# Kernel tuning notes

Hardware: AMD Instinct MI355X
Metric: run time of the kernel (lower is better)

The kernel has to match this reference:

```python
import jax, jax.numpy as jnp
import numpy as np

EPS = 1e-07      # epsilon from init kwargs
LRELU = 0.1      # LeakyReLU negative slope
LEVEL = 0        # level 0 -> _cond_inter: i%2!=0 and j%2!=0


def _conv_circ(x, w, b):
    # circular-padded 2D conv, NCHW / OIHW
    p = w.shape[-1] // 2
    x = jnp.pad(x, ((0, 0), (0, 0), (p, p), (p, p)), mode='wrap')
    y = jax.lax.conv_general_dilated(x, w, (1, 1), 'VALID',
                                     dimension_numbers=('NCHW', 'OIHW', 'NCHW'))
    return y + b[None, :, None, None]


def _net(x, w1, b1, w2, b2, w3, b3):
    h = jax.nn.leaky_relu(_conv_circ(x, w1, b1), LRELU)
    h = jax.nn.leaky_relu(_conv_circ(h, w2, b2), LRELU)
    return jax.nn.sigmoid(_conv_circ(h, w3, b3))


def _positions(L):
    ii, jj = np.meshgrid(np.arange(L), np.arange(L), indexing='ij')
    if LEVEL == 0:
        mask = (ii % 2 != 0) & (jj % 2 != 0)
    else:
        mask = ((ii % 2 == 0) & (jj % 2 != 0)) | ((ii % 2 != 0) & (jj % 2 == 0))
    # row-major order matches the nested python loop
    return jnp.asarray(np.stack([ii[mask], jj[mask]], axis=1), dtype=jnp.int32)  # [S,2]


def setup_inputs() -> dict:
    key = jax.random.key(0)
    ks = jax.random.split(key, 7)
    B, L, H, K = 4096, 16, 32, 5
    x = jnp.where(jax.random.normal(ks[0], (B, 1, L, L)) > 0, 1.0, -1.0).astype(jnp.float32)
    w1 = (jax.random.normal(ks[1], (H, 1, K, K)) * 0.1).astype(jnp.float32)
    b1 = jnp.zeros((H,), jnp.float32)
    w2 = (jax.random.normal(ks[2], (H, H, K, K)) * 0.05).astype(jnp.float32)
    b2 = jnp.zeros((H,), jnp.float32)
    w3 = (jax.random.normal(ks[3], (1, H, K, K)) * 0.05).astype(jnp.float32)
    b3 = jnp.zeros((1,), jnp.float32)
    return {'x': x, 'w1': w1, 'b1': b1, 'w2': w2, 'b2': b2, 'w3': w3, 'b3': b3}


def reference(x, w1, b1, w2, b2, w3, b3):
    B, L = x.shape[0], x.shape[-1]
    pos = _positions(L)                                   # [S,2] static positions
    keys = jax.random.split(jax.random.key(42), pos.shape[0])

    def step(carry, inp):
        x, logq = carry
        ij, k = inp
        i, j = ij[0], ij[1]
        x_hat = _net(x, w1, b1, w2, b2, w3, b3)           # full CNN pass per pixel
        p = x_hat[:, 0, i, j]                             # [B]
        samp = jax.lax.stop_gradient(
            jnp.where(jax.random.uniform(k, (B,)) < p, 1.0, -1.0))  # bernoulli*2-1
        x = x.at[:, 0, i, j].set(samp)
        xb = (samp + 1.0) * 0.5
        logq = logq + jnp.log(p + EPS) * xb + jnp.log(1.0 - p + EPS) * (1.0 - xb)
        return (x, logq), None

    (x, logq), _ = jax.lax.scan(step, (x, jnp.zeros((B,), x.dtype)), (pos, keys))
    return x, logq
```

## Files before the change

### kernel.cpp

```cpp
#include <hip/hip_runtime.h>
#include <cstdint>


struct U2 { uint32_t x, y; };

__device__ __forceinline__ U2 tf2x32(uint32_t k0, uint32_t k1, uint32_t x0, uint32_t x1) {
  uint32_t k2 = k0 ^ k1 ^ 0x1BD11BDAu;
#define TFROT(r) { x0 += x1; x1 = (x1 << (r)) | (x1 >> (32 - (r))); x1 ^= x0; }
  x0 += k0; x1 += k1;
  TFROT(13) TFROT(15) TFROT(26) TFROT(6)
  x0 += k1; x1 += k2 + 1u;
  TFROT(17) TFROT(29) TFROT(16) TFROT(24)
  x0 += k2; x1 += k0 + 2u;
  TFROT(13) TFROT(15) TFROT(26) TFROT(6)
  x0 += k0; x1 += k1 + 3u;
  TFROT(17) TFROT(29) TFROT(16) TFROT(24)
  x0 += k1; x1 += k2 + 4u;
  TFROT(13) TFROT(15) TFROT(26) TFROT(6)
  x0 += k2; x1 += k0 + 5u;
#undef TFROT
  return {x0, x1};
}

__device__ __forceinline__ float lrelu(float v) { return fmaxf(v, 0.1f * v); }

#define WOFF 4096

template<int CCH>
__device__ __forceinline__ void pb_accum(const float (&w2)[25], const float* h1d_ic,
                                         float (&acc)[27]) {
  #pragma unroll
  for (int dyp = 0; dyp < 5; ++dyp) {
    if (dyp + 4 < 3 * CCH || dyp + 4 > 3 * CCH + 6) continue;
    float h[5];
    #pragma unroll
    for (int dxp = 0; dxp < 5; ++dxp) h[dxp] = h1d_ic[(dyp * 5 + dxp) * 32];
    #pragma unroll
    for (int u2 = 0; u2 < 3; ++u2) {
      const int ky = dyp + 4 - 3 * CCH - u2;
      if (ky < 0 || ky > 4) continue;
      #pragma unroll
      for (int kx = 0; kx < 5; ++kx) {
        const float w = w2[ky * 5 + kx];
        #pragma unroll
        for (int dxp = 0; dxp < 5; ++dxp)
          acc[u2 * 9 + dxp - kx + 4] = fmaf(h[dxp], w, acc[u2 * 9 + dxp - kx + 4]);
      }
    }
  }
}

template<int CCH>
__device__ __forceinline__ void pb_chunk(const float (&w2a)[25], const float (&w2b)[25],
                                         int icp, const float* s_h1d, float* s_stage,
                                         float* s_a2, int tid, int lane, int wv,
                                         int i, int j) {
  float acc[27];
  #pragma unroll
  for (int q = 0; q < 27; ++q) acc[q] = 0.f;
  pb_accum<CCH>(w2a, s_h1d + icp, acc);
  pb_accum<CCH>(w2b, s_h1d + icp + 16, acc);
  #pragma unroll
  for (int q = 0; q < 27; ++q) acc[q] += __shfl_xor(acc[q], 32, 64);
  if (lane < 32) {
    #pragma unroll
    for (int q = 0; q < 27; ++q) s_stage[wv * 864 + q * 32 + lane] = acc[q];
  }
  __syncthreads();
  for (int e = tid; e < 864; e += 512) {
    float sm = 0.f;
    #pragma unroll
    for (int w = 0; w < 8; ++w) sm += s_stage[w * 864 + e];
    int q = e >> 5, o3 = e & 31;
    int u2 = q / 9, V = q - 9 * u2;
    int idx = (((i - 4 + 3 * CCH + u2) & 15) * 16 + ((j - 4 + V) & 15)) * 32 + o3;
    s_a2[idx] += sm;
  }
  __syncthreads();
}

__device__ __forceinline__ void init_conv2_half(const float (&w2)[25], int icc,
                                                const float* s_stage, float (&acc)[16]) {
  #pragma unroll
  for (int ky = 0; ky < 5; ++ky) {
    float h[16];
    #pragma unroll
    for (int col = 0; col < 16; ++col) h[col] = s_stage[WOFF + ky * 512 + col * 32 + icc];
    #pragma unroll
    for (int kx = 0; kx < 5; ++kx) {
      const float w = w2[ky * 5 + kx];
      #pragma unroll
      for (int X = 0; X < 16; ++X)
        acc[X] = fmaf(h[(X + kx - 2) & 15], w, acc[X]);
    }
  }
}

__launch_bounds__(512, 2)
__global__ void van_kernel(const float* __restrict__ gx,
                           const float* __restrict__ gw1, const float* __restrict__ gb1,
                           const float* __restrict__ gw2, const float* __restrict__ gb2,
                           const float* __restrict__ gw3, const float* __restrict__ gb3,
                           float* __restrict__ out, int B) {
  __shared__ __align__(16) float s_xf[784];
  __shared__ __align__(16) float s_w1[800];
  __shared__ float s_b1[32], s_b2[32];
  __shared__ float s_u[64];
  __shared__ float s_c3[8];
  __shared__ __align__(16) float s_h1d[800];
  __shared__ __align__(16) float s_a2[8192];
  __shared__ __align__(16) float s_stage[6912];

  const int tid  = threadIdx.x;
  const int bg   = blockIdx.x;
  const int lane = tid & 63;
  const int wv   = tid >> 6;
  const int oc   = tid & 31;
  const int icp  = tid >> 5;

  const float b3v = gb3[0];
  float w2a[25], w2b[25];
  {
    const float* pa = gw2 + (oc * 32 + icp) * 25;
    const float* pb = gw2 + (oc * 32 + icp + 16) * 25;
    #pragma unroll
    for (int k = 0; k < 25; ++k) { w2a[k] = pa[k]; w2b[k] = pb[k]; }
  }
  float w3r1 = gw3[(tid & 31) * 25 + (tid >> 5)];
  float w3r2 = 0.f;
  if (tid < 288) {
    int e = tid + 512;
    w3r2 = gw3[(e & 31) * 25 + (e >> 5)];
  }
  s_w1[tid] = gw1[tid];
  if (tid < 288) s_w1[tid + 512] = gw1[tid + 512];
  if (tid < 32)  { s_b1[tid] = gb1[tid]; s_b2[tid] = gb2[tid]; }
  {
    int rr = tid / 28, cc = tid - rr * 28;
    s_xf[tid] = gx[bg * 256 + ((rr - 6) & 15) * 16 + ((cc - 6) & 15)];
    if (tid < 272) {
      int t2 = tid + 512;
      int r2 = t2 / 28, c2 = t2 - r2 * 28;
      s_xf[t2] = gx[bg * 256 + ((r2 - 6) & 15) * 16 + ((c2 - 6) & 15)];
    }
  }
  if (tid < 64) {
    U2 key = tf2x32(0u, 42u, 0u, (uint32_t)tid);
    U2 tt  = tf2x32(key.x, key.y, 0u, (uint32_t)bg);
    uint32_t bits = tt.x ^ tt.y;
    s_u[tid] = __uint_as_float(0x3F800000u | (bits >> 9)) - 1.0f;
  }
  __syncthreads();

  #pragma unroll 1
  for (int t = 0; t < 16; ++t) {
    {
      const int colW = tid >> 5, icW = tid & 31;
      const float* wp = &s_w1[icW * 25];
      const float bb = s_b1[icW];
      #pragma unroll
      for (int r5 = 0; r5 < 5; ++r5) {
        int f = (t + r5 - 2) & 15;
        float a = bb;
        #pragma unroll
        for (int ky = 0; ky < 5; ++ky)
          #pragma unroll
          for (int kx = 0; kx < 5; ++kx)
            a = fmaf(s_xf[(f + 4 + ky) * 28 + colW + 4 + kx], wp[ky * 5 + kx], a);
        s_stage[WOFF + r5 * 512 + tid] = lrelu(a);
      }
    }
    __syncthreads();
    float acc[16];
    #pragma unroll
    for (int X = 0; X < 16; ++X) acc[X] = 0.f;
    init_conv2_half(w2a, icp, s_stage, acc);
    init_conv2_half(w2b, icp + 16, s_stage, acc);
    #pragma unroll
    for (int X = 0; X < 16; ++X) acc[X] += __shfl_xor(acc[X], 32, 64);
    if (lane < 32) {
      #pragma unroll
      for (int X = 0; X < 16; ++X) s_stage[wv * 512 + X * 32 + lane] = acc[X];
    }
    __syncthreads();
    {
      float sm = 0.f;
      #pragma unroll
      for (int w = 0; w < 8; ++w) sm += s_stage[w * 512 + tid];
      s_a2[t * 512 + tid] = sm + s_b2[tid & 31];
    }
    __syncthreads();
  }

  float logq = 0.f;
  #pragma unroll 1
  for (int s = 0; s < 64; ++s) {
    const int i = 2 * (s >> 3) + 1;
    const int j = 2 * (s & 7) + 1;

    float v3;
    {
      int p1 = tid >> 5, o1 = tid & 31;
      int dy = p1 / 5, dx = p1 - 5 * dy;
      int idx = (((i + dy - 2) & 15) * 16 + ((j + dx - 2) & 15)) * 32 + o1;
      v3 = lrelu(s_a2[idx]) * w3r1;
      if (tid < 288) {
        int e = tid + 512, p2 = e >> 5, o2 = e & 31;
        int dy2 = p2 / 5, dx2 = p2 - 5 * dy2;
        int idx2 = (((i + dy2 - 2) & 15) * 16 + ((j + dx2 - 2) & 15)) * 32 + o2;
        v3 = fmaf(lrelu(s_a2[idx2]), w3r2, v3);
      }
    }
    #pragma unroll
    for (int m = 32; m >= 1; m >>= 1) v3 += __shfl_xor(v3, m, 64);
    if (lane == 0) s_c3[wv] = v3;
    __syncthreads();

    float logit = b3v;
    #pragma unroll
    for (int v = 0; v < 8; ++v) logit += s_c3[v];
    const float pr   = 1.f / (1.f + expf(-logit));
    const float u    = s_u[s];
    const float samp = (u < pr) ? 1.f : -1.f;
    const float xold = s_xf[(i + 6) * 28 + (j + 6)];
    logq += (samp > 0.f) ? logf(pr + 1e-7f) : logf(1.f - pr + 1e-7f);

    if (samp == xold) { __syncthreads(); continue; }

    {
      const float delta = samp - xold;
      #pragma unroll
      for (int rep = 0; rep < 2; ++rep) {
        int e = tid + rep * 512;
        if (rep == 1 && tid >= 288) break;
        int p = e >> 5, icA = e & 31;
        int dyq = p / 5, dxq = p - 5 * dyq;
        const float* wp = &s_w1[icA * 25];
        float a1v = s_b1[icA];
        int base = (i + dyq + 2) * 28 + (j + dxq + 2);
        #pragma unroll
        for (int ky = 0; ky < 5; ++ky)
          #pragma unroll
          for (int kx = 0; kx < 5; ++kx)
            a1v = fmaf(s_xf[base + ky * 28 + kx], wp[ky * 5 + kx], a1v);
        float a1n = fmaf(delta, wp[(4 - dyq) * 5 + (4 - dxq)], a1v);
        s_h1d[p * 32 + icA] = lrelu(a1n) - lrelu(a1v);
      }
    }
    __syncthreads();

    if (tid == 511) {
      int r1 = i + 6, c1 = j + 6;
      int r2 = (i < 6) ? i + 22 : ((i >= 10) ? i - 10 : r1);
      int c2 = (j < 6) ? j + 22 : ((j >= 10) ? j - 10 : c1);
      s_xf[r1 * 28 + c1] = samp; s_xf[r1 * 28 + c2] = samp;
      s_xf[r2 * 28 + c1] = samp; s_xf[r2 * 28 + c2] = samp;
    }

    pb_chunk<0>(w2a, w2b, icp, s_h1d, s_stage, s_a2, tid, lane, wv, i, j);
    pb_chunk<1>(w2a, w2b, icp, s_h1d, s_stage, s_a2, tid, lane, wv, i, j);
    pb_chunk<2>(w2a, w2b, icp, s_h1d, s_stage, s_a2, tid, lane, wv, i, j);
  }

  if (tid < 256)
    out[bg * 256 + tid] = s_xf[((tid >> 4) + 6) * 28 + (tid & 15) + 6];
  if (tid == 0)
    out[B * 256 + bg] = logq;
}

extern "C" void kernel_launch(void* const* d_in, const int* in_sizes, int n_in,
                              void* d_out, int out_size, void* d_ws, size_t ws_size,
                              hipStream_t stream) {
  const float* gx  = (const float*)d_in[0];
  const float* gw1 = (const float*)d_in[1];
  const float* gb1 = (const float*)d_in[2];
  const float* gw2 = (const float*)d_in[3];
  const float* gb2 = (const float*)d_in[4];
  const float* gw3 = (const float*)d_in[5];
  const float* gb3 = (const float*)d_in[6];
  float* out = (float*)d_out;
  const int B = in_sizes[0] / 256;

  hipLaunchKernelGGL(van_kernel, dim3(B), dim3(512), 0, stream,
                     gx, gw1, gb1, gw2, gb2, gw3, gb3, out, B);
}
```

Before: 6.053 ms.

## Replace staged cross-wave reductions with LDS atomic adds and trim barriers

```diff
diff --git a/kernel.cpp b/kernel.cpp
--- a/kernel.cpp
+++ b/kernel.cpp
@@ -24,8 +24,6 @@
 
 __device__ __forceinline__ float lrelu(float v) { return fmaxf(v, 0.1f * v); }
 
-#define WOFF 4096
-
 template<int CCH>
 __device__ __forceinline__ void pb_accum(const float (&w2)[25], const float* h1d_ic,
                                          float (&acc)[27]) {
@@ -52,9 +50,8 @@
 
 template<int CCH>
 __device__ __forceinline__ void pb_chunk(const float (&w2a)[25], const float (&w2b)[25],
-                                         int icp, const float* s_h1d, float* s_stage,
-                                         float* s_a2, int tid, int lane, int wv,
-                                         int i, int j) {
+                                         int icp, const float* s_h1d, float* s_a2,
+                                         int lane, int i, int j) {
   float acc[27];
   #pragma unroll
   for (int q = 0; q < 27; ++q) acc[q] = 0.f;
@@ -64,28 +61,21 @@
   for (int q = 0; q < 27; ++q) acc[q] += __shfl_xor(acc[q], 32, 64);
   if (lane < 32) {
     #pragma unroll
-    for (int q = 0; q < 27; ++q) s_stage[wv * 864 + q * 32 + lane] = acc[q];
-  }
-  __syncthreads();
-  for (int e = tid; e < 864; e += 512) {
-    float sm = 0.f;
-    #pragma unroll
-    for (int w = 0; w < 8; ++w) sm += s_stage[w * 864 + e];
-    int q = e >> 5, o3 = e & 31;
-    int u2 = q / 9, V = q - 9 * u2;
-    int idx = (((i - 4 + 3 * CCH + u2) & 15) * 16 + ((j - 4 + V) & 15)) * 32 + o3;
-    s_a2[idx] += sm;
-  }
-  __syncthreads();
+    for (int q = 0; q < 27; ++q) {
+      const int u2 = q / 9, V = q - 9 * u2;
+      int idx = (((i - 4 + 3 * CCH + u2) & 15) * 16 + ((j - 4 + V) & 15)) * 32 + lane;
+      atomicAdd(&s_a2[idx], acc[q]);
+    }
+  }
 }
 
 __device__ __forceinline__ void init_conv2_half(const float (&w2)[25], int icc,
-                                                const float* s_stage, float (&acc)[16]) {
+                                                const float* s_win, float (&acc)[16]) {
   #pragma unroll
   for (int ky = 0; ky < 5; ++ky) {
     float h[16];
     #pragma unroll
-    for (int col = 0; col < 16; ++col) h[col] = s_stage[WOFF + ky * 512 + col * 32 + icc];
+    for (int col = 0; col < 16; ++col) h[col] = s_win[ky * 512 + col * 32 + icc];
     #pragma unroll
     for (int kx = 0; kx < 5; ++kx) {
       const float w = w2[ky * 5 + kx];
@@ -106,10 +96,10 @@
   __shared__ __align__(16) float s_w1[800];
   __shared__ float s_b1[32], s_b2[32];
   __shared__ float s_u[64];
-  __shared__ float s_c3[8];
+  __shared__ float s_c3[2][8];
   __shared__ __align__(16) float s_h1d[800];
   __shared__ __align__(16) float s_a2[8192];
-  __shared__ __align__(16) float s_stage[6912];
+  __shared__ __align__(16) float s_win[2560];
 
   const int tid  = threadIdx.x;
   const int bg   = blockIdx.x;
@@ -150,6 +140,8 @@
     uint32_t bits = tt.x ^ tt.y;
     s_u[tid] = __uint_as_float(0x3F800000u | (bits >> 9)) - 1.0f;
   }
+  #pragma unroll
+  for (int k = 0; k < 16; ++k) s_a2[k * 512 + tid] = gb2[tid & 31];
   __syncthreads();
 
   #pragma unroll 1
@@ -167,27 +159,20 @@
           #pragma unroll
           for (int kx = 0; kx < 5; ++kx)
             a = fmaf(s_xf[(f + 4 + ky) * 28 + colW + 4 + kx], wp[ky * 5 + kx], a);
-        s_stage[WOFF + r5 * 512 + tid] = lrelu(a);
+        s_win[r5 * 512 + tid] = lrelu(a);
       }
     }
     __syncthreads();
     float acc[16];
     #pragma unroll
     for (int X = 0; X < 16; ++X) acc[X] = 0.f;
-    init_conv2_half(w2a, icp, s_stage, acc);
-    init_conv2_half(w2b, icp + 16, s_stage, acc);
+    init_conv2_half(w2a, icp, s_win, acc);
+    init_conv2_half(w2b, icp + 16, s_win, acc);
     #pragma unroll
     for (int X = 0; X < 16; ++X) acc[X] += __shfl_xor(acc[X], 32, 64);
     if (lane < 32) {
       #pragma unroll
-      for (int X = 0; X < 16; ++X) s_stage[wv * 512 + X * 32 + lane] = acc[X];
-    }
-    __syncthreads();
-    {
-      float sm = 0.f;
-      #pragma unroll
-      for (int w = 0; w < 8; ++w) sm += s_stage[w * 512 + tid];
-      s_a2[t * 512 + tid] = sm + s_b2[tid & 31];
+      for (int X = 0; X < 16; ++X) atomicAdd(&s_a2[t * 512 + X * 32 + lane], acc[X]);
     }
     __syncthreads();
   }
@@ -197,6 +182,7 @@
   for (int s = 0; s < 64; ++s) {
     const int i = 2 * (s >> 3) + 1;
     const int j = 2 * (s & 7) + 1;
+    const int par = s & 1;
 
     float v3;
     {
@@ -213,19 +199,19 @@
     }
     #pragma unroll
     for (int m = 32; m >= 1; m >>= 1) v3 += __shfl_xor(v3, m, 64);
-    if (lane == 0) s_c3[wv] = v3;
+    if (lane == 0) s_c3[par][wv] = v3;
     __syncthreads();
 
     float logit = b3v;
     #pragma unroll
-    for (int v = 0; v < 8; ++v) logit += s_c3[v];
+    for (int v = 0; v < 8; ++v) logit += s_c3[par][v];
     const float pr   = 1.f / (1.f + expf(-logit));
     const float u    = s_u[s];
     const float samp = (u < pr) ? 1.f : -1.f;
     const float xold = s_xf[(i + 6) * 28 + (j + 6)];
     logq += (samp > 0.f) ? logf(pr + 1e-7f) : logf(1.f - pr + 1e-7f);
 
-    if (samp == xold) { __syncthreads(); continue; }
+    if (samp == xold) continue;
 
     {
       const float delta = samp - xold;
@@ -257,9 +243,10 @@
       s_xf[r2 * 28 + c1] = samp; s_xf[r2 * 28 + c2] = samp;
     }
 
-    pb_chunk<0>(w2a, w2b, icp, s_h1d, s_stage, s_a2, tid, lane, wv, i, j);
-    pb_chunk<1>(w2a, w2b, icp, s_h1d, s_stage, s_a2, tid, lane, wv, i, j);
-    pb_chunk<2>(w2a, w2b, icp, s_h1d, s_stage, s_a2, tid, lane, wv, i, j);
+    pb_chunk<0>(w2a, w2b, icp, s_h1d, s_a2, lane, i, j);
+    pb_chunk<1>(w2a, w2b, icp, s_h1d, s_a2, lane, i, j);
+    pb_chunk<2>(w2a, w2b, icp, s_h1d, s_a2, lane, i, j);
+    __syncthreads();
   }
 
   if (tid < 256)
```

Result: slower. 20.84 ms (+244.3%).
